# Kernel tuning notes

Measured on AMD Instinct MI355X. Metric: run time of the kernel, lower is better.

The kernel has to match this reference:

```python
import jax, jax.numpy as jnp
import numpy as np
from jax import lax

# Paraformer-large streaming decoder dims
L, H, DFF, NH, DK, K, V, T, S, CKV, LB = 16, 512, 2048, 4, 128, 11, 8404, 64, 2048, 256, 256


def _ln(x, g, b, eps=1e-5):
    m = jnp.mean(x, axis=-1, keepdims=True)
    var = jnp.mean((x - m) ** 2, axis=-1, keepdims=True)
    return (x - m) * lax.rsqrt(var + eps) * g + b


def setup_inputs() -> dict:
    key = jax.random.key(0)
    ks = jax.random.split(key, 20)
    w = lambda k, shp: jax.random.normal(k, shp, jnp.float32) * 0.02
    return {
        "encoder_out": jax.random.normal(ks[0], (1, S, H), jnp.float32),
        "list_frame": jax.random.normal(ks[1], (1, T, H), jnp.float32),
        "fsmn_cache": jax.random.normal(ks[2], (L, 1, H, K - 1), jnp.float32),
        "key_cache": jax.random.normal(ks[3], (L, NH, DK, CKV), jnp.float32),
        "value_cache": jax.random.normal(ks[4], (L, NH, CKV, DK), jnp.float32),
        "norm1_g": jnp.ones((L, H)), "norm1_b": jnp.zeros((L, H)),
        "norm2_g": jnp.ones((L, H)), "norm2_b": jnp.zeros((L, H)),
        "norm3_g": jnp.ones((L, H)), "norm3_b": jnp.zeros((L, H)),
        "ffn_norm_g": jnp.ones((L, DFF)), "ffn_norm_b": jnp.zeros((L, DFF)),
        "w1": w(ks[5], (L, H, DFF)), "b1": jnp.zeros((L, DFF)),
        "w2": w(ks[6], (L, DFF, H)),  # bias-free in FunASR DecoderSANM
        "fsmn_w": w(ks[7], (L, H, K)),  # depthwise conv, groups=H, no bias
        "qw": w(ks[8], (L, H, H)), "qb": jnp.zeros((L, H)),
        "kvw": w(ks[9], (L, H, 2 * H)), "kvb": jnp.zeros((L, 2 * H)),
        "ow": w(ks[10], (L, H, H)), "ob": jnp.zeros((L, H)),
        "d3_norm1_g": jnp.ones((H,)), "d3_norm1_b": jnp.zeros((H,)),
        "d3_w1": w(ks[11], (H, DFF)), "d3_b1": jnp.zeros((DFF,)),
        "d3_ffn_norm_g": jnp.ones((DFF,)), "d3_ffn_norm_b": jnp.zeros((DFF,)),
        "d3_w2": w(ks[12], (DFF, H)),
        "after_norm_g": jnp.ones((H,)), "after_norm_b": jnp.zeros((H,)),
        "out_w": w(ks[13], (H, V)), "out_b": jnp.zeros((V,)),
        "list_frame_len": T,
    }


def reference(encoder_out, list_frame, fsmn_cache, key_cache, value_cache,
              norm1_g, norm1_b, norm2_g, norm2_b, norm3_g, norm3_b,
              ffn_norm_g, ffn_norm_b, w1, b1, w2, fsmn_w, qw, qb, kvw, kvb, ow, ob,
              d3_norm1_g, d3_norm1_b, d3_w1, d3_b1, d3_ffn_norm_g, d3_ffn_norm_b, d3_w2,
              after_norm_g, after_norm_b, out_w, out_b, list_frame_len):
    enc = encoder_out[0]  # [S, H]
    scale = DK ** -0.5

    def layer_fn(lf, p):
        (fc, kc, vc, n1g, n1b, n2g, n2b, n3g, n3b, fng, fnb,
         W1, B1, W2, FW, QW, QB, KVW, KVB, OW, OB) = p
        residual = lf
        y = _ln(lf, n1g, n1b)
        y = _ln(jax.nn.relu(y @ W1 + B1), fng, fnb) @ W2
        y = _ln(y, n2g, n2b)
        # cache concat; slice [look_back:] with look_back = -(K-1)-T keeps all K-1+T cols
        x_cat = jnp.concatenate([fc, jnp.swapaxes(y, 1, 2)], axis=-1)  # [1, H, K-1+T]
        conv = lax.conv_general_dilated(
            x_cat, FW[:, None, :], (1,), 'VALID',
            dimension_numbers=('NCH', 'OIH', 'NCH'), feature_group_count=H)  # [1, H, T]
        x = jnp.swapaxes(conv, 1, 2) + y + residual
        residual = x
        q = (_ln(x, n3g, n3b)[0] @ QW + QB).reshape(-1, NH, DK).transpose(1, 0, 2) * scale  # [h, T, dk]
        kv = enc @ KVW + KVB  # [S, 2H]
        k = kv[:, :H].reshape(-1, NH, DK).transpose(1, 2, 0)  # [h, dk, S]
        v = kv[:, H:].reshape(-1, NH, DK).transpose(1, 0, 2)  # [h, S, dk]
        k = jnp.concatenate([kc, k], axis=2)  # [h, dk, CKV+S]
        v = jnp.concatenate([vc, v], axis=1)  # [h, CKV+S, dk]
        attn = jax.nn.softmax(jnp.einsum('htd,hds->hts', q, k), axis=-1)
        ctx = jnp.einsum('hts,hsd->htd', attn, v).transpose(1, 0, 2).reshape(1, -1, H)
        lf = residual + ctx @ OW + OB
        return lf, (x_cat, k[:, :, -LB:], v[:, -LB:, :])

    layer_params = (fsmn_cache, key_cache, value_cache, norm1_g, norm1_b, norm2_g, norm2_b,
                    norm3_g, norm3_b, ffn_norm_g, ffn_norm_b, w1, b1, w2, fsmn_w,
                    qw, qb, kvw, kvb, ow, ob)
    lf, (save_fsmn, save_keys, save_values) = lax.scan(layer_fn, list_frame, layer_params)
    x = _ln(lf, d3_norm1_g, d3_norm1_b)
    x = _ln(jax.nn.relu(x @ d3_w1 + d3_b1), d3_ffn_norm_g, d3_ffn_norm_b) @ d3_w2
    logits = _ln(x, after_norm_g, after_norm_b) @ out_w + out_b
    max_logit_ids = jnp.argmax(logits, axis=-1).astype(jnp.int32)
    return save_fsmn, save_keys, save_values, max_logit_ids
```

## Files before the change

kernel.cpp:

```cpp
#include <hip/hip_runtime.h>

constexpr int LAY = 16, HID = 512, FF = 2048, NHD = 4, DKH = 128, KW = 11,
              VOC = 8404, TT = 64, SEQ = 2048, LBN = 256;

#define SWZ(row, e) ((e) ^ ((((row) >> 2) & 7) << 2))

__global__ void diag_k(float* __restrict__ p, float v) { p[threadIdx.x] = v; }

__global__ __launch_bounds__(256) void redln_k(
    const float* __restrict__ P, int N, int nch,
    const float* __restrict__ bias, const float* __restrict__ res, int relu,
    const float* __restrict__ g, const float* __restrict__ b,
    float* __restrict__ out1, float* __restrict__ out2) {
  __shared__ float buf[2048];
  __shared__ float red[256];
  const int m = blockIdx.x, tid = threadIdx.x;
  float s = 0.f;
  for (int n = tid; n < N; n += 256) {
    const float* p = P + (size_t)m * N + n;
    float v = 0.f;
    for (int c = 0; c < nch; ++c) v += p[(size_t)c * 64 * N];
    if (bias) v += bias[n];
    if (res) v += res[(size_t)m * N + n];
    if (relu) v = fmaxf(v, 0.f);
    if (out1) out1[(size_t)m * N + n] = v;
    buf[n] = v; s += v;
  }
  red[tid] = s; __syncthreads();
  for (int st = 128; st > 0; st >>= 1) { if (tid < st) red[tid] += red[tid + st]; __syncthreads(); }
  const float mean = red[0] / N;
  __syncthreads();
  float vs = 0.f;
  for (int n = tid; n < N; n += 256) { float d = buf[n] - mean; vs += d * d; }
  red[tid] = vs; __syncthreads();
  for (int st = 128; st > 0; st >>= 1) { if (tid < st) red[tid] += red[tid + st]; __syncthreads(); }
  const float inv = rsqrtf(red[0] / N + 1e-5f);
  for (int n = tid; n < N; n += 256)
    out2[(size_t)m * N + n] = (buf[n] - mean) * inv * g[n] + b[n];
}

__global__ __launch_bounds__(256) void gemm_nn(
    const float* __restrict__ A, int lda, long sA,
    const float* __restrict__ B, int ldb, long sB,
    float* __restrict__ C, int ldc, long sC,
    const float* __restrict__ bias,
    const float* __restrict__ res, int ldres,
    int N, int Kd, int flags, int nch,
    float* __restrict__ part, long pzs, int coff,
    int aCh, long aChS) {
  __shared__ float As[64][64];
  __shared__ float Bs[64][64];
  const int tid = threadIdx.x;
  const int lr = tid >> 4, lc = tid & 15;
  const int bn = blockIdx.x * 64;
  const int chunk = blockIdx.y;
  const int z = blockIdx.z;
  A += (long)z * sA; B += (long)z * sB; C += (long)z * sC;
  float acc[4][4] = {};
  const int ktiles = Kd >> 6;
  const int fa = (lc & 7) << 2;
  for (int kt = chunk; kt < ktiles; kt += nch) {
    const int k0 = kt << 6;
    __syncthreads();
#pragma unroll
    for (int i = 0; i < 4; ++i) {
      const int r = lr + 16 * i;
      const float* ap = A + (size_t)r * lda + k0 + lc * 4;
      float4 av = *(const float4*)ap;
      for (int c = 1; c < aCh; ++c) {
        const float4 t2 = *(const float4*)(ap + (size_t)c * aChS);
        av.x += t2.x; av.y += t2.y; av.z += t2.z; av.w += t2.w;
      }
      As[lc * 4 + 0][r ^ fa] = av.x; As[lc * 4 + 1][r ^ fa] = av.y;
      As[lc * 4 + 2][r ^ fa] = av.z; As[lc * 4 + 3][r ^ fa] = av.w;
      const int n = bn + lc * 4;
      const float* bp = B + (size_t)(k0 + r) * ldb + n;
      float4 bv;
      if (n + 3 < N) bv = *(const float4*)bp;
      else {
        bv.x = (n + 0 < N) ? bp[0] : 0.f;
        bv.y = (n + 1 < N) ? bp[1] : 0.f;
        bv.z = (n + 2 < N) ? bp[2] : 0.f;
        bv.w = (n + 3 < N) ? bp[3] : 0.f;
      }
      *(float4*)(&Bs[r][SWZ(r, lc * 4)]) = bv;
    }
    __syncthreads();
#pragma unroll 8
    for (int kk = 0; kk < 64; ++kk) {
      const int fk = ((kk >> 2) & 7) << 2;
      const float4 a = *(const float4*)(&As[kk][(lr * 4) ^ fk]);
      const float4 b = *(const float4*)(&Bs[kk][(lc * 4) ^ fk]);
      acc[0][0] += a.x * b.x; acc[0][1] += a.x * b.y; acc[0][2] += a.x * b.z; acc[0][3] += a.x * b.w;
      acc[1][0] += a.y * b.x; acc[1][1] += a.y * b.y; acc[1][2] += a.y * b.z; acc[1][3] += a.y * b.w;
      acc[2][0] += a.z * b.x; acc[2][1] += a.z * b.y; acc[2][2] += a.z * b.z; acc[2][3] += a.z * b.w;
      acc[3][0] += a.w * b.x; acc[3][1] += a.w * b.y; acc[3][2] += a.w * b.z; acc[3][3] += a.w * b.w;
    }
  }
  if (part) {
    float* P = part + (size_t)z * pzs + (size_t)(coff + chunk) * 64 * N;
#pragma unroll
    for (int i = 0; i < 4; ++i) {
      const int m = lr * 4 + i;
#pragma unroll
      for (int j = 0; j < 4; ++j) P[(size_t)m * N + bn + lc * 4 + j] = acc[i][j];
    }
    return;
  }
#pragma unroll
  for (int i = 0; i < 4; ++i) {
    const int m = lr * 4 + i;
#pragma unroll
    for (int j = 0; j < 4; ++j) {
      const int n = bn + lc * 4 + j;
      if (n < N) {
        float v = acc[i][j];
        if (bias) v += bias[n];
        if (res) v += res[(size_t)m * ldres + n];
        if (flags & 2) v += C[(size_t)m * ldc + n];
        if (flags & 1) v = fmaxf(v, 0.f);
        C[(size_t)m * ldc + n] = v;
      }
    }
  }
}

__global__ __launch_bounds__(256) void red_k(
    const float* __restrict__ P, float* __restrict__ out,
    int N, int nch, long pzs, int outld, int zoff,
    const float* __restrict__ bias, const float* __restrict__ res,
    const float* __restrict__ rsv, const float* __restrict__ bvv,
    int relu, int total) {
  const int idx = blockIdx.x * 256 + threadIdx.x;
  if (idx >= total) return;
  const int z = idx / (64 * N);
  const int rem = idx - z * 64 * N;
  const int t = rem / N;
  const int n = rem - t * N;
  const float* p = P + (size_t)z * pzs + (size_t)t * N + n;
  float s = 0.f;
  for (int c = 0; c < nch; ++c) s += p[(size_t)c * 64 * N];
  const int oc = z * zoff + n;
  if (bias) s += bias[oc];
  if (res) s += res[(size_t)t * outld + oc];
  if (rsv) s += rsv[z * 64 + t] * bvv[oc];
  if (relu) s = fmaxf(s, 0.f);
  out[(size_t)t * outld + oc] = s;
}

__global__ __launch_bounds__(256) void gemm_nt(
    const float* __restrict__ A, int lda, long sA,
    const float* __restrict__ B, int ldb, long sB,
    float* __restrict__ C, int ldc, long sC,
    int N, int Kd, int nch, float* __restrict__ part) {
  __shared__ float As[64][64];
  __shared__ float Bs[64][64];
  const int tid = threadIdx.x;
  const int lr = tid >> 4, lc = tid & 15;
  const int bn = blockIdx.x * 64;
  const int chunk = blockIdx.y;
  const int z = blockIdx.z;
  A += (long)z * sA; B += (long)z * sB; C += (long)z * sC;
  float acc[4][4] = {};
  const int ktiles = Kd >> 6;
  const int fa = (lc & 7) << 2;
  for (int kt = chunk; kt < ktiles; kt += nch) {
    const int k0 = kt << 6;
    __syncthreads();
#pragma unroll
    for (int i = 0; i < 4; ++i) {
      const int r = lr + 16 * i;
      const float4 av = *(const float4*)(A + (size_t)r * lda + k0 + lc * 4);
      As[lc * 4 + 0][r ^ fa] = av.x; As[lc * 4 + 1][r ^ fa] = av.y;
      As[lc * 4 + 2][r ^ fa] = av.z; As[lc * 4 + 3][r ^ fa] = av.w;
      const float4 bv = *(const float4*)(B + (size_t)(bn + r) * ldb + k0 + lc * 4);
      Bs[lc * 4 + 0][r ^ fa] = bv.x; Bs[lc * 4 + 1][r ^ fa] = bv.y;
      Bs[lc * 4 + 2][r ^ fa] = bv.z; Bs[lc * 4 + 3][r ^ fa] = bv.w;
    }
    __syncthreads();
#pragma unroll 8
    for (int kk = 0; kk < 64; ++kk) {
      const int fk = ((kk >> 2) & 7) << 2;
      const float4 a = *(const float4*)(&As[kk][(lr * 4) ^ fk]);
      const float4 b = *(const float4*)(&Bs[kk][(lc * 4) ^ fk]);
      acc[0][0] += a.x * b.x; acc[0][1] += a.x * b.y; acc[0][2] += a.x * b.z; acc[0][3] += a.x * b.w;
      acc[1][0] += a.y * b.x; acc[1][1] += a.y * b.y; acc[1][2] += a.y * b.z; acc[1][3] += a.y * b.w;
      acc[2][0] += a.z * b.x; acc[2][1] += a.z * b.y; acc[2][2] += a.z * b.z; acc[2][3] += a.z * b.w;
      acc[3][0] += a.w * b.x; acc[3][1] += a.w * b.y; acc[3][2] += a.w * b.z; acc[3][3] += a.w * b.w;
    }
  }
  if (chunk == 0) {
#pragma unroll
    for (int i = 0; i < 4; ++i)
#pragma unroll
      for (int j = 0; j < 4; ++j)
        C[(size_t)(lr * 4 + i) * ldc + bn + lc * 4 + j] = acc[i][j];
  } else {
    float* P = part + (size_t)z * (64L * SEQ) + (size_t)(chunk - 1) * 64 * SEQ * NHD;
#pragma unroll
    for (int i = 0; i < 4; ++i)
#pragma unroll
      for (int j = 0; j < 4; ++j)
        P[(size_t)(lr * 4 + i) * SEQ + bn + lc * 4 + j] = acc[i][j];
  }
}

__global__ __launch_bounds__(256) void attn1_k(
    const float* __restrict__ qpart, const float* __restrict__ qbi_l,
    const float* __restrict__ Wkv, const float* __restrict__ kcl,
    float* __restrict__ qp, float* __restrict__ sc,
    int ckv, int sct) {
  __shared__ float As[64][64];
  __shared__ float Bs[64][64];
  const int tid = threadIdx.x;
  const int lr = tid >> 4, lc = tid & 15;
  const int h = blockIdx.z;
  const bool isQp = blockIdx.x < 8;
  const int bn = (isQp ? blockIdx.x : blockIdx.x - 8) * 64;
  const int fa = (lc & 7) << 2;
  float acc[4][4] = {};
  for (int k0 = 0; k0 < DKH; k0 += 64) {
    __syncthreads();
#pragma unroll
    for (int i = 0; i < 4; ++i) {
      const int r = lr + 16 * i;
      const float* ap = qpart + (size_t)r * HID + h * DKH + k0 + lc * 4;
      float4 av = *(const float4*)ap;
      for (int c = 1; c < 8; ++c) {
        const float4 t2 = *(const float4*)(ap + (size_t)c * 64 * HID);
        av.x += t2.x; av.y += t2.y; av.z += t2.z; av.w += t2.w;
      }
      const float4 bb = *(const float4*)(qbi_l + h * DKH + k0 + lc * 4);
      av.x += bb.x; av.y += bb.y; av.z += bb.z; av.w += bb.w;
      As[lc * 4 + 0][r ^ fa] = av.x; As[lc * 4 + 1][r ^ fa] = av.y;
      As[lc * 4 + 2][r ^ fa] = av.z; As[lc * 4 + 3][r ^ fa] = av.w;
      if (isQp) {
        const float4 bv = *(const float4*)(Wkv + (size_t)(bn + r) * (2 * HID) + h * DKH + k0 + lc * 4);
        Bs[lc * 4 + 0][r ^ fa] = bv.x; Bs[lc * 4 + 1][r ^ fa] = bv.y;
        Bs[lc * 4 + 2][r ^ fa] = bv.z; Bs[lc * 4 + 3][r ^ fa] = bv.w;
      } else {
        const float4 bv = *(const float4*)(kcl + ((size_t)h * DKH + k0 + r) * ckv + bn + lc * 4);
        *(float4*)(&Bs[r][SWZ(r, lc * 4)]) = bv;
      }
    }
    __syncthreads();
#pragma unroll 8
    for (int kk = 0; kk < 64; ++kk) {
      const int fk = ((kk >> 2) & 7) << 2;
      const float4 a = *(const float4*)(&As[kk][(lr * 4) ^ fk]);
      const float4 b = *(const float4*)(&Bs[kk][(lc * 4) ^ fk]);
      acc[0][0] += a.x * b.x; acc[0][1] += a.x * b.y; acc[0][2] += a.x * b.z; acc[0][3] += a.x * b.w;
      acc[1][0] += a.y * b.x; acc[1][1] += a.y * b.y; acc[1][2] += a.y * b.z; acc[1][3] += a.y * b.w;
      acc[2][0] += a.z * b.x; acc[2][1] += a.z * b.y; acc[2][2] += a.z * b.z; acc[2][3] += a.z * b.w;
      acc[3][0] += a.w * b.x; acc[3][1] += a.w * b.y; acc[3][2] += a.w * b.z; acc[3][3] += a.w * b.w;
    }
  }
  if (isQp) {
    float* C = qp + (size_t)h * TT * HID;
#pragma unroll
    for (int i = 0; i < 4; ++i)
#pragma unroll
      for (int j = 0; j < 4; ++j)
        C[(size_t)(lr * 4 + i) * HID + bn + lc * 4 + j] = acc[i][j];
  } else {
    float* C = sc + (size_t)h * TT * sct;
#pragma unroll
    for (int i = 0; i < 4; ++i)
#pragma unroll
      for (int j = 0; j < 4; ++j)
        C[(size_t)(lr * 4 + i) * sct + bn + lc * 4 + j] = acc[i][j];
  }
}

__global__ __launch_bounds__(256) void attn2_k(
    const float* __restrict__ sc, const float* __restrict__ vcl,
    const float* __restrict__ enc,
    float* __restrict__ part, float* __restrict__ partE,
    int ckv, int sct, int ncho, long pzc) {
  __shared__ float As[64][64];
  __shared__ float Bs[64][64];
  const int tid = threadIdx.x;
  const int lr = tid >> 4, lc = tid & 15;
  const int h = blockIdx.z;
  const int by = blockIdx.y;
  const bool isOld = blockIdx.x < 2;
  if (isOld && by >= ncho) return;
  if (!isOld && by >= 8) return;
  const float* A;
  const float* Bb;
  int lda, ldb, N, ktiles, nch, bn;
  float* P;
  if (isOld) {
    A = sc + (size_t)h * TT * sct;  lda = sct;
    Bb = vcl + (size_t)h * ckv * DKH; ldb = DKH;
    N = DKH; ktiles = ckv >> 6; nch = ncho; bn = blockIdx.x * 64;
    P = part + (size_t)h * pzc + (size_t)by * 64 * DKH;
  } else {
    A = sc + ckv + (size_t)h * TT * sct; lda = sct;
    Bb = enc; ldb = HID;
    N = HID; ktiles = SEQ >> 6; nch = 8; bn = (blockIdx.x - 2) * 64;
    P = partE + (size_t)h * (8L * 64 * HID) + (size_t)by * 64 * HID;
  }
  const int fa = (lc & 7) << 2;
  float acc[4][4] = {};
  for (int kt = by; kt < ktiles; kt += nch) {
    const int k0 = kt << 6;
    __syncthreads();
#pragma unroll
    for (int i = 0; i < 4; ++i) {
      const int r = lr + 16 * i;
      const float4 av = *(const float4*)(A + (size_t)r * lda + k0 + lc * 4);
      As[lc * 4 + 0][r ^ fa] = av.x; As[lc * 4 + 1][r ^ fa] = av.y;
      As[lc * 4 + 2][r ^ fa] = av.z; As[lc * 4 + 3][r ^ fa] = av.w;
      const float4 bv = *(const float4*)(Bb + (size_t)(k0 + r) * ldb + bn + lc * 4);
      *(float4*)(&Bs[r][SWZ(r, lc * 4)]) = bv;
    }
    __syncthreads();
#pragma unroll 8
    for (int kk = 0; kk < 64; ++kk) {
      const int fk = ((kk >> 2) & 7) << 2;
      const float4 a = *(const float4*)(&As[kk][(lr * 4) ^ fk]);
      const float4 b = *(const float4*)(&Bs[kk][(lc * 4) ^ fk]);
      acc[0][0] += a.x * b.x; acc[0][1] += a.x * b.y; acc[0][2] += a.x * b.z; acc[0][3] += a.x * b.w;
      acc[1][0] += a.y * b.x; acc[1][1] += a.y * b.y; acc[1][2] += a.y * b.z; acc[1][3] += a.y * b.w;
      acc[2][0] += a.z * b.x; acc[2][1] += a.z * b.y; acc[2][2] += a.z * b.z; acc[2][3] += a.z * b.w;
      acc[3][0] += a.w * b.x; acc[3][1] += a.w * b.y; acc[3][2] += a.w * b.z; acc[3][3] += a.w * b.w;
    }
  }
#pragma unroll
  for (int i = 0; i < 4; ++i)
#pragma unroll
    for (int j = 0; j < 4; ++j)
      P[(size_t)(lr * 4 + i) * N + bn + lc * 4 + j] = acc[i][j];
}

__global__ __launch_bounds__(256) void fsmnln_k(
    const float* __restrict__ y4, const float* __restrict__ lfin,
    const float* __restrict__ cache, const float* __restrict__ fw,
    const float* __restrict__ g, const float* __restrict__ b,
    float* __restrict__ xb, float* __restrict__ xcat,
    float* __restrict__ y1out) {
  __shared__ float buf[HID];
  __shared__ float red[256];
  const int t = blockIdx.x, tid = threadIdx.x;
  float s = 0.f;
  for (int h = tid; h < HID; h += 256) {
    float conv = 0.f;
#pragma unroll
    for (int k = 0; k < KW; ++k) {
      const int j = t + k;
      const float xcv = (j < KW - 1) ? cache[h * (KW - 1) + j]
                                     : y4[(size_t)(j - (KW - 1)) * HID + h];
      conv += xcv * fw[h * KW + k];
    }
    const float yv = y4[(size_t)t * HID + h];
    const float x = conv + yv + lfin[(size_t)t * HID + h];
    xb[(size_t)t * HID + h] = x;
    buf[h] = x; s += x;
    xcat[h * (KW - 1 + TT) + (KW - 1) + t] = yv;
    if (t == 0) {
      for (int j2 = 0; j2 < KW - 1; ++j2)
        xcat[h * (KW - 1 + TT) + j2] = cache[h * (KW - 1) + j2];
    }
  }
  red[tid] = s; __syncthreads();
  for (int st = 128; st > 0; st >>= 1) { if (tid < st) red[tid] += red[tid + st]; __syncthreads(); }
  const float mean = red[0] / HID;
  __syncthreads();
  float vs = 0.f;
  for (int h = tid; h < HID; h += 256) { float d = buf[h] - mean; vs += d * d; }
  red[tid] = vs; __syncthreads();
  for (int st = 128; st > 0; st >>= 1) { if (tid < st) red[tid] += red[tid + st]; __syncthreads(); }
  const float inv = rsqrtf(red[0] / HID + 1e-5f);
  for (int h = tid; h < HID; h += 256)
    y1out[(size_t)t * HID + h] = (buf[h] - mean) * inv * g[h] + b[h];
}

__global__ __launch_bounds__(256) void softmax_k(
    float* __restrict__ sc, float* __restrict__ rs,
    const float* __restrict__ qpart, const float* __restrict__ qbi_l,
    const float* __restrict__ kb, const float* __restrict__ partN,
    int cols, int newStart, float alpha) {
  __shared__ float srow[8192];
  __shared__ float red[256];
  const int tid = threadIdx.x;
  const int row = blockIdx.x;
  const int h = row >> 6, t = row & 63;
  sc += (size_t)row * cols;
  const float* pn = partN + (size_t)h * 64 * SEQ + (size_t)t * SEQ;
  float qv = 0.f;
  if (tid < DKH) {
    const float* qp0 = qpart + (size_t)t * HID + h * DKH + tid;
    float q = qp0[0];
    for (int c = 1; c < 8; ++c) q += qp0[(size_t)c * 64 * HID];
    q += qbi_l[h * DKH + tid];
    qv = q * kb[h * DKH + tid];
  }
  red[tid] = qv; __syncthreads();
  for (int st = 64; st > 0; st >>= 1) { if (tid < st) red[tid] += red[tid + st]; __syncthreads(); }
  const float qcv = red[0];
  __syncthreads();
  float m = -3.4e38f;
  for (int c = tid; c < cols; c += 256) {
    float v = sc[c];
    if (c >= newStart) v += pn[c - newStart] + qcv;
    v *= alpha;
    srow[c] = v; m = fmaxf(m, v);
  }
  red[tid] = m; __syncthreads();
  for (int st = 128; st > 0; st >>= 1) { if (tid < st) red[tid] = fmaxf(red[tid], red[tid + st]); __syncthreads(); }
  m = red[0]; __syncthreads();
  float s = 0.f;
  for (int c = tid; c < cols; c += 256) {
    const float e = __expf(srow[c] - m);
    srow[c] = e; s += e;
  }
  red[tid] = s; __syncthreads();
  for (int st = 128; st > 0; st >>= 1) { if (tid < st) red[tid] += red[tid + st]; __syncthreads(); }
  const float inv = 1.f / red[0];
  float ns = 0.f;
  for (int c = tid; c < cols; c += 256) {
    const float p = srow[c] * inv; sc[c] = p;
    if (c >= newStart) ns += p;
  }
  __syncthreads();
  red[tid] = ns; __syncthreads();
  for (int st = 128; st > 0; st >>= 1) { if (tid < st) red[tid] += red[tid + st]; __syncthreads(); }
  if (tid == 0) rs[row] = red[0];
}

__global__ __launch_bounds__(256) void argmax_k(const float* __restrict__ lg,
                                                float* __restrict__ out) {
  __shared__ float vs[256];
  __shared__ int ix[256];
  const int tid = threadIdx.x;
  lg += (size_t)blockIdx.x * VOC;
  float bm = -3.4e38f;
  int bi = 0;
  for (int c = tid; c < VOC; c += 256) { float v = lg[c]; if (v > bm) { bm = v; bi = c; } }
  vs[tid] = bm; ix[tid] = bi; __syncthreads();
  for (int st = 128; st > 0; st >>= 1) {
    if (tid < st) {
      if (vs[tid + st] > vs[tid] || (vs[tid + st] == vs[tid] && ix[tid + st] < ix[tid])) {
        vs[tid] = vs[tid + st]; ix[tid] = ix[tid + st];
      }
    }
    __syncthreads();
  }
  if (tid == 0) out[blockIdx.x] = (float)ix[0];
}

__global__ __launch_bounds__(256) void kvsave_k(const float* __restrict__ enc,
                                                const float* __restrict__ kvw,
                                                const float* __restrict__ kvb,
                                                float* __restrict__ keys,
                                                float* __restrict__ vals) {
  __shared__ float As[64][64];
  __shared__ float Bs[64][64];
  const int tid = threadIdx.x;
  const int lr = tid >> 4, lc = tid & 15;
  const int bn = blockIdx.x * 64, bm = blockIdx.y * 64;
  const int l = blockIdx.z;
  const float* W = kvw + (size_t)l * HID * 2 * HID;
  const int fa = (lc & 7) << 2;
  float acc[4][4] = {};
  for (int k0 = 0; k0 < HID; k0 += 64) {
    __syncthreads();
#pragma unroll
    for (int i = 0; i < 4; ++i) {
      const int r = lr + 16 * i;
      const float4 av =
          *(const float4*)(enc + (size_t)(SEQ - LBN + bm + r) * HID + k0 + lc * 4);
      As[lc * 4 + 0][r ^ fa] = av.x; As[lc * 4 + 1][r ^ fa] = av.y;
      As[lc * 4 + 2][r ^ fa] = av.z; As[lc * 4 + 3][r ^ fa] = av.w;
      const float4 bv = *(const float4*)(W + (size_t)(k0 + r) * (2 * HID) + bn + lc * 4);
      *(float4*)(&Bs[r][SWZ(r, lc * 4)]) = bv;
    }
    __syncthreads();
#pragma unroll 8
    for (int kk = 0; kk < 64; ++kk) {
      const int fk = ((kk >> 2) & 7) << 2;
      const float4 a = *(const float4*)(&As[kk][(lr * 4) ^ fk]);
      const float4 b = *(const float4*)(&Bs[kk][(lc * 4) ^ fk]);
      acc[0][0] += a.x * b.x; acc[0][1] += a.x * b.y; acc[0][2] += a.x * b.z; acc[0][3] += a.x * b.w;
      acc[1][0] += a.y * b.x; acc[1][1] += a.y * b.y; acc[1][2] += a.y * b.z; acc[1][3] += a.y * b.w;
      acc[2][0] += a.z * b.x; acc[2][1] += a.z * b.y; acc[2][2] += a.z * b.z; acc[2][3] += a.z * b.w;
      acc[3][0] += a.w * b.x; acc[3][1] += a.w * b.y; acc[3][2] += a.w * b.z; acc[3][3] += a.w * b.w;
    }
  }
#pragma unroll
  for (int i = 0; i < 4; ++i) {
    const int m = bm + lr * 4 + i;
#pragma unroll
    for (int j = 0; j < 4; ++j) {
      const int n = bn + lc * 4 + j;
      const float v = acc[i][j] + kvb[(size_t)l * 2 * HID + n];
      if (n < 512) {
        const int h = n >> 7, d = n & 127;
        keys[(((size_t)l * NHD + h) * DKH + d) * LBN + m] = v;
      } else {
        const int c = n - 512, h = c >> 7, d = c & 127;
        vals[(((size_t)l * NHD + h) * LBN + m) * DKH + d] = v;
      }
    }
  }
}

extern "C" void kernel_launch(void* const* d_in, const int* in_sizes, int n_in,
                              void* d_out, int out_size, void* d_ws, size_t ws_size,
                              hipStream_t stream) {
  static const int EXPECT[34] = {
      1048576, 32768, 81920, -1, -1,
      8192, 8192, 8192, 8192, 8192, 8192,
      32768, 32768,
      16777216, 32768, 16777216, 90112,
      4194304, 8192, 8388608, 16384, 4194304, 8192,
      512, 512, 1048576, 2048, 2048, 2048, 1048576,
      512, 512, 4302848, 8404};
  if (out_size != 4800576) {
    diag_k<<<1, 64, 0, stream>>>((float*)d_out, 9800000.f);
    return;
  }
  float* out_fsmn = (float*)d_out;
  float* out_keys = out_fsmn + (size_t)LAY * HID * (KW - 1 + TT);
  float* out_vals = out_keys + (size_t)LAY * NHD * DKH * LBN;
  float* out_ids  = out_vals + (size_t)LAY * NHD * LBN * DKH;
  if (n_in < 34) {
    diag_k<<<1, 64, 0, stream>>>(out_ids, 9900000.f);
    return;
  }
  for (int i = 0; i < 34; ++i) {
    if (EXPECT[i] >= 0 && in_sizes[i] != EXPECT[i]) {
      diag_k<<<1, 64, 0, stream>>>(out_ids, (float)((i + 1) * 100000));
      return;
    }
  }
  const long per = (long)LAY * NHD * DKH;
  const long ckl = (long)in_sizes[3] / per;
  if ((long)in_sizes[3] != ckl * per || in_sizes[4] != in_sizes[3] ||
      ckl <= 0 || (ckl & 63) != 0 || ckl > 6144) {
    diag_k<<<1, 64, 0, stream>>>(out_fsmn, (float)in_sizes[3]);
    return;
  }
  if (ws_size < (size_t)3145728 * 4) {
    diag_k<<<1, 64, 0, stream>>>(out_fsmn, 1.0e6f + (float)(ws_size >> 20));
    return;
  }
  const int ckv = (int)ckl;
  const int sct = ckv + SEQ;
  const long TS = (long)TT * sct;
  const int ncho = (ckv / 64 < 8) ? (ckv / 64) : 8;

  const float* enc    = (const float*)d_in[0];
  const float* lfrm   = (const float*)d_in[1];
  const float* fcache = (const float*)d_in[2];
  const float* kcache = (const float*)d_in[3];
  const float* vcache = (const float*)d_in[4];
  const float* n1g = (const float*)d_in[5];  const float* n1b = (const float*)d_in[6];
  const float* n2g = (const float*)d_in[7];  const float* n2b = (const float*)d_in[8];
  const float* n3g = (const float*)d_in[9];  const float* n3b = (const float*)d_in[10];
  const float* fng = (const float*)d_in[11]; const float* fnb = (const float*)d_in[12];
  const float* w1  = (const float*)d_in[13]; const float* b1  = (const float*)d_in[14];
  const float* w2  = (const float*)d_in[15];
  const float* fw  = (const float*)d_in[16];
  const float* qw  = (const float*)d_in[17]; const float* qbi  = (const float*)d_in[18];
  const float* kvw = (const float*)d_in[19]; const float* kvbi = (const float*)d_in[20];
  const float* ow  = (const float*)d_in[21]; const float* obi  = (const float*)d_in[22];
  const float* d3n1g = (const float*)d_in[23]; const float* d3n1b = (const float*)d_in[24];
  const float* d3w1  = (const float*)d_in[25]; const float* d3b1  = (const float*)d_in[26];
  const float* d3fng = (const float*)d_in[27]; const float* d3fnb = (const float*)d_in[28];
  const float* d3w2  = (const float*)d_in[29];
  const float* ang   = (const float*)d_in[30]; const float* anb = (const float*)d_in[31];
  const float* outw  = (const float*)d_in[32]; const float* outb = (const float*)d_in[33];

  float* sc  = out_keys;
  float* ov  = out_vals;
  float* lf  = ov + 0;
  float* y1  = ov + 32768;
  float* y4  = ov + 98304;
  float* xb  = ov + 131072;
  float* ctx = ov + 196608;
  float* y2  = ov + 360448;
  float* qp  = ov + 491520;
  float* rs  = ov + 753920;
  float* lg  = ov + 754176;
  float* wsf   = (float*)d_ws;
  float* part  = wsf;
  float* partE = wsf + 1048576;
  float* partN = wsf + 2097152;

  const float alpha = 0.08838834764831845f;
  const long TH = (long)TT * HID;
  const long pz_ctx = (long)(ncho + 4) * 64 * DKH;

  redln_k<<<TT, 256, 0, stream>>>(lfrm, HID, 1, nullptr, nullptr, 0,
                                  n1g, n1b, lf, y1);

  for (int l = 0; l < LAY; ++l) {
    const float* Wkv = kvw + (size_t)l * HID * 2 * HID;
    const float* Bkv = kvbi + (size_t)l * 2 * HID;
    const float* qbi_l = qbi + (size_t)l * HID;
    gemm_nn<<<dim3(32, 8, 1), 256, 0, stream>>>(
        y1, HID, 0, w1 + (size_t)l * HID * FF, FF, 0, nullptr, 0, 0,
        nullptr, nullptr, 0, FF, HID, 0, 8, part, 0, 0, 1, 0);
    redln_k<<<TT, 256, 0, stream>>>(part, FF, 8, b1 + (size_t)l * FF, nullptr, 1,
                                    fng + (size_t)l * FF, fnb + (size_t)l * FF,
                                    nullptr, y2);
    gemm_nn<<<dim3(8, 32, 1), 256, 0, stream>>>(
        y2, FF, 0, w2 + (size_t)l * FF * HID, HID, 0, nullptr, 0, 0,
        nullptr, nullptr, 0, HID, FF, 0, 32, part, 0, 0, 1, 0);
    redln_k<<<TT, 256, 0, stream>>>(part, HID, 32, nullptr, nullptr, 0,
                                    n2g + l * HID, n2b + l * HID, nullptr, y4);
    fsmnln_k<<<TT, 256, 0, stream>>>(y4, lf, fcache + (size_t)l * HID * (KW - 1),
                                     fw + (size_t)l * HID * KW,
                                     n3g + l * HID, n3b + l * HID,
                                     xb, out_fsmn + (size_t)l * HID * (KW - 1 + TT), y1);
    gemm_nn<<<dim3(8, 8, 1), 256, 0, stream>>>(
        y1, HID, 0, qw + (size_t)l * HID * HID, HID, 0, nullptr, 0, 0,
        nullptr, nullptr, 0, HID, HID, 0, 8, part, 0, 0, 1, 0);
    attn1_k<<<dim3(8 + ckv / 64, 1, NHD), 256, 0, stream>>>(
        part, qbi_l, Wkv, kcache + (size_t)l * NHD * DKH * ckv, qp, sc, ckv, sct);
    gemm_nt<<<dim3(32, 2, NHD), 256, 0, stream>>>(
        qp, HID, TH, enc, HID, 0, sc + ckv, sct, TS, SEQ, HID, 2, partN);
    softmax_k<<<NHD * TT, 256, 0, stream>>>(sc, rs, part, qbi_l, Bkv, partN,
                                            sct, ckv, alpha);
    attn2_k<<<dim3(10, 8, NHD), 256, 0, stream>>>(
        sc, vcache + (size_t)l * NHD * ckv * DKH, enc, part, partE,
        ckv, sct, ncho, pz_ctx);
    gemm_nn<<<dim3(2, 4, NHD), 256, 0, stream>>>(
        partE, HID, 8L * 64 * HID, Wkv + HID, 2 * HID, DKH, nullptr, 0, 0,
        nullptr, nullptr, 0, DKH, HID, 0, 4, part, pz_ctx, ncho, 8, 64L * HID);
    red_k<<<128, 256, 0, stream>>>(part, ctx, DKH, ncho + 4, pz_ctx, HID, DKH,
                                   nullptr, nullptr, rs, Bkv + HID, 0, NHD * TT * DKH);
    gemm_nn<<<dim3(8, 8, 1), 256, 0, stream>>>(
        ctx, HID, 0, ow + (size_t)l * HID * HID, HID, 0, nullptr, 0, 0,
        nullptr, nullptr, 0, HID, HID, 0, 8, part, 0, 0, 1, 0);
    const float* ng = (l + 1 < LAY) ? n1g + (l + 1) * HID : d3n1g;
    const float* nb = (l + 1 < LAY) ? n1b + (l + 1) * HID : d3n1b;
    redln_k<<<TT, 256, 0, stream>>>(part, HID, 8, obi + (size_t)l * HID, xb, 0,
                                    ng, nb, lf, y1);
  }

  gemm_nn<<<dim3(32, 8, 1), 256, 0, stream>>>(
      y1, HID, 0, d3w1, FF, 0, nullptr, 0, 0, nullptr, nullptr, 0,
      FF, HID, 0, 8, part, 0, 0, 1, 0);
  redln_k<<<TT, 256, 0, stream>>>(part, FF, 8, d3b1, nullptr, 1,
                                  d3fng, d3fnb, nullptr, y2);
  gemm_nn<<<dim3(8, 32, 1), 256, 0, stream>>>(
      y2, FF, 0, d3w2, HID, 0, nullptr, 0, 0, nullptr, nullptr, 0,
      HID, FF, 0, 32, part, 0, 0, 1, 0);
  redln_k<<<TT, 256, 0, stream>>>(part, HID, 32, nullptr, nullptr, 0,
                                  ang, anb, nullptr, y4);
  gemm_nn<<<dim3((VOC + 63) / 64, 1, 1), 256, 0, stream>>>(
      y4, HID, 0, outw, VOC, 0, lg, VOC, 0, outb, nullptr, 0,
      VOC, HID, 0, 1, nullptr, 0, 0, 1, 0);
  argmax_k<<<TT, 256, 0, stream>>>(lg, out_ids);

  kvsave_k<<<dim3(2 * HID / 64, LBN / 64, LAY), 256, 0, stream>>>(
      enc, kvw, kvbi, out_keys, out_vals);
}
```

Measured before the change: 3.015 ms.

## Pack four independent 256-thread tiles into each 1024-thread block

Each kernel now launches blocks of 256x4 threads. Every threadIdx.y slice works on its own tile, chunk or row with private shared memory, and grids shrink by four. This cuts the number of blocks scheduled, perhaps to fit an occupancy or dispatch pattern. Shared memory per block grows to 128KB for the GEMM kernels, which may limit residency to one block per CU. The __syncthreads calls now span all four slices, so each slice waits on the others. A dedicated gemm_vx is added for the vocab projection, and the unused res and flags paths are removed.

```diff
diff --git a/kernel.cpp b/kernel.cpp
--- a/kernel.cpp
+++ b/kernel.cpp
@@ -7,14 +7,15 @@
 
 __global__ void diag_k(float* __restrict__ p, float v) { p[threadIdx.x] = v; }
 
-__global__ __launch_bounds__(256) void redln_k(
+__global__ __launch_bounds__(1024) void redln_k(
     const float* __restrict__ P, int N, int nch,
     const float* __restrict__ bias, const float* __restrict__ res, int relu,
     const float* __restrict__ g, const float* __restrict__ b,
     float* __restrict__ out1, float* __restrict__ out2) {
-  __shared__ float buf[2048];
-  __shared__ float red[256];
-  const int m = blockIdx.x, tid = threadIdx.x;
+  __shared__ float buf[4][2048];
+  __shared__ float red[4][256];
+  const int ty = threadIdx.y, tid = threadIdx.x;
+  const int m = blockIdx.x * 4 + ty;
   float s = 0.f;
   for (int n = tid; n < N; n += 256) {
     const float* p = P + (size_t)m * N + n;
@@ -24,36 +25,37 @@
     if (res) v += res[(size_t)m * N + n];
     if (relu) v = fmaxf(v, 0.f);
     if (out1) out1[(size_t)m * N + n] = v;
-    buf[n] = v; s += v;
-  }
-  red[tid] = s; __syncthreads();
-  for (int st = 128; st > 0; st >>= 1) { if (tid < st) red[tid] += red[tid + st]; __syncthreads(); }
-  const float mean = red[0] / N;
+    buf[ty][n] = v; s += v;
+  }
+  red[ty][tid] = s; __syncthreads();
+  for (int st = 128; st > 0; st >>= 1) { if (tid < st) red[ty][tid] += red[ty][tid + st]; __syncthreads(); }
+  const float mean = red[ty][0] / N;
   __syncthreads();
   float vs = 0.f;
-  for (int n = tid; n < N; n += 256) { float d = buf[n] - mean; vs += d * d; }
-  red[tid] = vs; __syncthreads();
-  for (int st = 128; st > 0; st >>= 1) { if (tid < st) red[tid] += red[tid + st]; __syncthreads(); }
-  const float inv = rsqrtf(red[0] / N + 1e-5f);
+  for (int n = tid; n < N; n += 256) { float d = buf[ty][n] - mean; vs += d * d; }
+  red[ty][tid] = vs; __syncthreads();
+  for (int st = 128; st > 0; st >>= 1) { if (tid < st) red[ty][tid] += red[ty][tid + st]; __syncthreads(); }
+  const float inv = rsqrtf(red[ty][0] / N + 1e-5f);
   for (int n = tid; n < N; n += 256)
-    out2[(size_t)m * N + n] = (buf[n] - mean) * inv * g[n] + b[n];
-}
-
-__global__ __launch_bounds__(256) void gemm_nn(
+    out2[(size_t)m * N + n] = (buf[ty][n] - mean) * inv * g[n] + b[n];
+}
+
+__global__ __launch_bounds__(1024) void gemm_nn(
     const float* __restrict__ A, int lda, long sA,
     const float* __restrict__ B, int ldb, long sB,
     float* __restrict__ C, int ldc, long sC,
     const float* __restrict__ bias,
-    const float* __restrict__ res, int ldres,
     int N, int Kd, int flags, int nch,
     float* __restrict__ part, long pzs, int coff,
     int aCh, long aChS) {
-  __shared__ float As[64][64];
-  __shared__ float Bs[64][64];
-  const int tid = threadIdx.x;
+  __shared__ float As[4][64][64];
+  __shared__ float Bs[4][64][64];
+  const int ty = threadIdx.y, tid = threadIdx.x;
   const int lr = tid >> 4, lc = tid & 15;
   const int bn = blockIdx.x * 64;
-  const int chunk = blockIdx.y;
+  int chunk = blockIdx.y * 4 + ty;
+  const int valid = chunk < nch;
+  if (!valid) chunk = nch - 1;
   const int z = blockIdx.z;
   A += (long)z * sA; B += (long)z * sB; C += (long)z * sC;
   float acc[4][4] = {};
@@ -71,8 +73,8 @@
         const float4 t2 = *(const float4*)(ap + (size_t)c * aChS);
         av.x += t2.x; av.y += t2.y; av.z += t2.z; av.w += t2.w;
       }
-      As[lc * 4 + 0][r ^ fa] = av.x; As[lc * 4 + 1][r ^ fa] = av.y;
-      As[lc * 4 + 2][r ^ fa] = av.z; As[lc * 4 + 3][r ^ fa] = av.w;
+      As[ty][lc * 4 + 0][r ^ fa] = av.x; As[ty][lc * 4 + 1][r ^ fa] = av.y;
+      As[ty][lc * 4 + 2][r ^ fa] = av.z; As[ty][lc * 4 + 3][r ^ fa] = av.w;
       const int n = bn + lc * 4;
       const float* bp = B + (size_t)(k0 + r) * ldb + n;
       float4 bv;
@@ -83,20 +85,21 @@
         bv.z = (n + 2 < N) ? bp[2] : 0.f;
         bv.w = (n + 3 < N) ? bp[3] : 0.f;
       }
-      *(float4*)(&Bs[r][SWZ(r, lc * 4)]) = bv;
+      *(float4*)(&Bs[ty][r][SWZ(r, lc * 4)]) = bv;
     }
     __syncthreads();
 #pragma unroll 8
     for (int kk = 0; kk < 64; ++kk) {
       const int fk = ((kk >> 2) & 7) << 2;
-      const float4 a = *(const float4*)(&As[kk][(lr * 4) ^ fk]);
-      const float4 b = *(const float4*)(&Bs[kk][(lc * 4) ^ fk]);
+      const float4 a = *(const float4*)(&As[ty][kk][(lr * 4) ^ fk]);
+      const float4 b = *(const float4*)(&Bs[ty][kk][(lc * 4) ^ fk]);
       acc[0][0] += a.x * b.x; acc[0][1] += a.x * b.y; acc[0][2] += a.x * b.z; acc[0][3] += a.x * b.w;
       acc[1][0] += a.y * b.x; acc[1][1] += a.y * b.y; acc[1][2] += a.y * b.z; acc[1][3] += a.y * b.w;
       acc[2][0] += a.z * b.x; acc[2][1] += a.z * b.y; acc[2][2] += a.z * b.z; acc[2][3] += a.z * b.w;
       acc[3][0] += a.w * b.x; acc[3][1] += a.w * b.y; acc[3][2] += a.w * b.z; acc[3][3] += a.w * b.w;
     }
   }
+  if (!valid) return;
   if (part) {
     float* P = part + (size_t)z * pzs + (size_t)(coff + chunk) * 64 * N;
 #pragma unroll
@@ -116,8 +119,6 @@
       if (n < N) {
         float v = acc[i][j];
         if (bias) v += bias[n];
-        if (res) v += res[(size_t)m * ldres + n];
-        if (flags & 2) v += C[(size_t)m * ldc + n];
         if (flags & 1) v = fmaxf(v, 0.f);
         C[(size_t)m * ldc + n] = v;
       }
@@ -125,13 +126,70 @@
   }
 }
 
-__global__ __launch_bounds__(256) void red_k(
+__global__ __launch_bounds__(1024) void gemm_vx(
+    const float* __restrict__ A, int lda,
+    const float* __restrict__ B, int ldb,
+    float* __restrict__ C, int ldc,
+    const float* __restrict__ bias, int N, int Kd, int ntx) {
+  __shared__ float As[4][64][64];
+  __shared__ float Bs[4][64][64];
+  const int ty = threadIdx.y, tid = threadIdx.x;
+  const int lr = tid >> 4, lc = tid & 15;
+  int tile = blockIdx.x * 4 + ty;
+  const int valid = tile < ntx;
+  if (!valid) tile = 0;
+  const int bn = tile * 64;
+  const int fa = (lc & 7) << 2;
+  float acc[4][4] = {};
+  for (int k0 = 0; k0 < Kd; k0 += 64) {
+    __syncthreads();
+#pragma unroll
+    for (int i = 0; i < 4; ++i) {
+      const int r = lr + 16 * i;
+      const float4 av = *(const float4*)(A + (size_t)r * lda + k0 + lc * 4);
+      As[ty][lc * 4 + 0][r ^ fa] = av.x; As[ty][lc * 4 + 1][r ^ fa] = av.y;
+      As[ty][lc * 4 + 2][r ^ fa] = av.z; As[ty][lc * 4 + 3][r ^ fa] = av.w;
+      const int n = bn + lc * 4;
+      const float* bp = B + (size_t)(k0 + r) * ldb + n;
+      float4 bv;
+      if (n + 3 < N) bv = *(const float4*)bp;
+      else {
+        bv.x = (n + 0 < N) ? bp[0] : 0.f;
+        bv.y = (n + 1 < N) ? bp[1] : 0.f;
+        bv.z = (n + 2 < N) ? bp[2] : 0.f;
+        bv.w = (n + 3 < N) ? bp[3] : 0.f;
+      }
+      *(float4*)(&Bs[ty][r][SWZ(r, lc * 4)]) = bv;
+    }
+    __syncthreads();
+#pragma unroll 8
+    for (int kk = 0; kk < 64; ++kk) {
+      const int fk = ((kk >> 2) & 7) << 2;
+      const float4 a = *(const float4*)(&As[ty][kk][(lr * 4) ^ fk]);
+      const float4 b = *(const float4*)(&Bs[ty][kk][(lc * 4) ^ fk]);
+      acc[0][0] += a.x * b.x; acc[0][1] += a.x * b.y; acc[0][2] += a.x * b.z; acc[0][3] += a.x * b.w;
+      acc[1][0] += a.y * b.x; acc[1][1] += a.y * b.y; acc[1][2] += a.y * b.z; acc[1][3] += a.y * b.w;
+      acc[2][0] += a.z * b.x; acc[2][1] += a.z * b.y; acc[2][2] += a.z * b.z; acc[2][3] += a.z * b.w;
+      acc[3][0] += a.w * b.x; acc[3][1] += a.w * b.y; acc[3][2] += a.w * b.z; acc[3][3] += a.w * b.w;
+    }
+  }
+  if (!valid) return;
+#pragma unroll
+  for (int i = 0; i < 4; ++i) {
+    const int m = lr * 4 + i;
+#pragma unroll
+    for (int j = 0; j < 4; ++j) {
+      const int n = bn + lc * 4 + j;
+      if (n < N) C[(size_t)m * ldc + n] = acc[i][j] + bias[n];
+    }
+  }
+}
+
+__global__ __launch_bounds__(1024) void red_k(
     const float* __restrict__ P, float* __restrict__ out,
     int N, int nch, long pzs, int outld, int zoff,
-    const float* __restrict__ bias, const float* __restrict__ res,
-    const float* __restrict__ rsv, const float* __restrict__ bvv,
-    int relu, int total) {
-  const int idx = blockIdx.x * 256 + threadIdx.x;
+    const float* __restrict__ rsv, const float* __restrict__ bvv, int total) {
+  const int idx = blockIdx.x * 1024 + threadIdx.x;
   if (idx >= total) return;
   const int z = idx / (64 * N);
   const int rem = idx - z * 64 * N;
@@ -141,23 +199,23 @@
   float s = 0.f;
   for (int c = 0; c < nch; ++c) s += p[(size_t)c * 64 * N];
   const int oc = z * zoff + n;
-  if (bias) s += bias[oc];
-  if (res) s += res[(size_t)t * outld + oc];
   if (rsv) s += rsv[z * 64 + t] * bvv[oc];
-  if (relu) s = fmaxf(s, 0.f);
   out[(size_t)t * outld + oc] = s;
 }
 
-__global__ __launch_bounds__(256) void gemm_nt(
+__global__ __launch_bounds__(1024) void gemm_nt(
     const float* __restrict__ A, int lda, long sA,
     const float* __restrict__ B, int ldb, long sB,
     float* __restrict__ C, int ldc, long sC,
     int N, int Kd, int nch, float* __restrict__ part) {
-  __shared__ float As[64][64];
-  __shared__ float Bs[64][64];
-  const int tid = threadIdx.x;
+  __shared__ float As[4][64][64];
+  __shared__ float Bs[4][64][64];
+  const int ty = threadIdx.y, tid = threadIdx.x;
   const int lr = tid >> 4, lc = tid & 15;
-  const int bn = blockIdx.x * 64;
+  int tile = blockIdx.x * 4 + ty;
+  const int valid = tile * 64 < N;
+  if (!valid) tile = 0;
+  const int bn = tile * 64;
   const int chunk = blockIdx.y;
   const int z = blockIdx.z;
   A += (long)z * sA; B += (long)z * sB; C += (long)z * sC;
@@ -171,24 +229,25 @@
     for (int i = 0; i < 4; ++i) {
       const int r = lr + 16 * i;
       const float4 av = *(const float4*)(A + (size_t)r * lda + k0 + lc * 4);
-      As[lc * 4 + 0][r ^ fa] = av.x; As[lc * 4 + 1][r ^ fa] = av.y;
-      As[lc * 4 + 2][r ^ fa] = av.z; As[lc * 4 + 3][r ^ fa] = av.w;
+      As[ty][lc * 4 + 0][r ^ fa] = av.x; As[ty][lc * 4 + 1][r ^ fa] = av.y;
+      As[ty][lc * 4 + 2][r ^ fa] = av.z; As[ty][lc * 4 + 3][r ^ fa] = av.w;
       const float4 bv = *(const float4*)(B + (size_t)(bn + r) * ldb + k0 + lc * 4);
-      Bs[lc * 4 + 0][r ^ fa] = bv.x; Bs[lc * 4 + 1][r ^ fa] = bv.y;
-      Bs[lc * 4 + 2][r ^ fa] = bv.z; Bs[lc * 4 + 3][r ^ fa] = bv.w;
+      Bs[ty][lc * 4 + 0][r ^ fa] = bv.x; Bs[ty][lc * 4 + 1][r ^ fa] = bv.y;
+      Bs[ty][lc * 4 + 2][r ^ fa] = bv.z; Bs[ty][lc * 4 + 3][r ^ fa] = bv.w;
     }
     __syncthreads();
 #pragma unroll 8
     for (int kk = 0; kk < 64; ++kk) {
       const int fk = ((kk >> 2) & 7) << 2;
-      const float4 a = *(const float4*)(&As[kk][(lr * 4) ^ fk]);
-      const float4 b = *(const float4*)(&Bs[kk][(lc * 4) ^ fk]);
+      const float4 a = *(const float4*)(&As[ty][kk][(lr * 4) ^ fk]);
+      const float4 b = *(const float4*)(&Bs[ty][kk][(lc * 4) ^ fk]);
       acc[0][0] += a.x * b.x; acc[0][1] += a.x * b.y; acc[0][2] += a.x * b.z; acc[0][3] += a.x * b.w;
       acc[1][0] += a.y * b.x; acc[1][1] += a.y * b.y; acc[1][2] += a.y * b.z; acc[1][3] += a.y * b.w;
       acc[2][0] += a.z * b.x; acc[2][1] += a.z * b.y; acc[2][2] += a.z * b.z; acc[2][3] += a.z * b.w;
       acc[3][0] += a.w * b.x; acc[3][1] += a.w * b.y; acc[3][2] += a.w * b.z; acc[3][3] += a.w * b.w;
     }
   }
+  if (!valid) return;
   if (chunk == 0) {
 #pragma unroll
     for (int i = 0; i < 4; ++i)
@@ -205,18 +264,21 @@
   }
 }
 
-__global__ __launch_bounds__(256) void attn1_k(
+__global__ __launch_bounds__(1024) void attn1_k(
     const float* __restrict__ qpart, const float* __restrict__ qbi_l,
     const float* __restrict__ Wkv, const float* __restrict__ kcl,
     float* __restrict__ qp, float* __restrict__ sc,
     int ckv, int sct) {
-  __shared__ float As[64][64];
-  __shared__ float Bs[64][64];
-  const int tid = threadIdx.x;
+  __shared__ float As[4][64][64];
+  __shared__ float Bs[4][64][64];
+  const int ty = threadIdx.y, tid = threadIdx.x;
   const int lr = tid >> 4, lc = tid & 15;
   const int h = blockIdx.z;
-  const bool isQp = blockIdx.x < 8;
-  const int bn = (isQp ? blockIdx.x : blockIdx.x - 8) * 64;
+  int tile = blockIdx.x * 4 + ty;
+  const int valid = tile < 8 + ckv / 64;
+  if (!valid) tile = 0;
+  const bool isQp = tile < 8;
+  const int bn = (isQp ? tile : tile - 8) * 64;
   const int fa = (lc & 7) << 2;
   float acc[4][4] = {};
   for (int k0 = 0; k0 < DKH; k0 += 64) {
@@ -232,29 +294,30 @@
       }
       const float4 bb = *(const float4*)(qbi_l + h * DKH + k0 + lc * 4);
       av.x += bb.x; av.y += bb.y; av.z += bb.z; av.w += bb.w;
-      As[lc * 4 + 0][r ^ fa] = av.x; As[lc * 4 + 1][r ^ fa] = av.y;
-      As[lc * 4 + 2][r ^ fa] = av.z; As[lc * 4 + 3][r ^ fa] = av.w;
+      As[ty][lc * 4 + 0][r ^ fa] = av.x; As[ty][lc * 4 + 1][r ^ fa] = av.y;
+      As[ty][lc * 4 + 2][r ^ fa] = av.z; As[ty][lc * 4 + 3][r ^ fa] = av.w;
       if (isQp) {
         const float4 bv = *(const float4*)(Wkv + (size_t)(bn + r) * (2 * HID) + h * DKH + k0 + lc * 4);
-        Bs[lc * 4 + 0][r ^ fa] = bv.x; Bs[lc * 4 + 1][r ^ fa] = bv.y;
-        Bs[lc * 4 + 2][r ^ fa] = bv.z; Bs[lc * 4 + 3][r ^ fa] = bv.w;
+        Bs[ty][lc * 4 + 0][r ^ fa] = bv.x; Bs[ty][lc * 4 + 1][r ^ fa] = bv.y;
+        Bs[ty][lc * 4 + 2][r ^ fa] = bv.z; Bs[ty][lc * 4 + 3][r ^ fa] = bv.w;
       } else {
         const float4 bv = *(const float4*)(kcl + ((size_t)h * DKH + k0 + r) * ckv + bn + lc * 4);
-        *(float4*)(&Bs[r][SWZ(r, lc * 4)]) = bv;
+        *(float4*)(&Bs[ty][r][SWZ(r, lc * 4)]) = bv;
       }
     }
     __syncthreads();
 #pragma unroll 8
     for (int kk = 0; kk < 64; ++kk) {
       const int fk = ((kk >> 2) & 7) << 2;
-      const float4 a = *(const float4*)(&As[kk][(lr * 4) ^ fk]);
-      const float4 b = *(const float4*)(&Bs[kk][(lc * 4) ^ fk]);
+      const float4 a = *(const float4*)(&As[ty][kk][(lr * 4) ^ fk]);
+      const float4 b = *(const float4*)(&Bs[ty][kk][(lc * 4) ^ fk]);
       acc[0][0] += a.x * b.x; acc[0][1] += a.x * b.y; acc[0][2] += a.x * b.z; acc[0][3] += a.x * b.w;
       acc[1][0] += a.y * b.x; acc[1][1] += a.y * b.y; acc[1][2] += a.y * b.z; acc[1][3] += a.y * b.w;
       acc[2][0] += a.z * b.x; acc[2][1] += a.z * b.y; acc[2][2] += a.z * b.z; acc[2][3] += a.z * b.w;
       acc[3][0] += a.w * b.x; acc[3][1] += a.w * b.y; acc[3][2] += a.w * b.z; acc[3][3] += a.w * b.w;
     }
   }
+  if (!valid) return;
   if (isQp) {
     float* C = qp + (size_t)h * TT * HID;
 #pragma unroll
@@ -272,35 +335,39 @@
   }
 }
 
-__global__ __launch_bounds__(256) void attn2_k(
+__global__ __launch_bounds__(1024) void attn2_k(
     const float* __restrict__ sc, const float* __restrict__ vcl,
     const float* __restrict__ enc,
     float* __restrict__ part, float* __restrict__ partE,
     int ckv, int sct, int ncho, long pzc) {
-  __shared__ float As[64][64];
-  __shared__ float Bs[64][64];
-  const int tid = threadIdx.x;
+  __shared__ float As[4][64][64];
+  __shared__ float Bs[4][64][64];
+  const int ty = threadIdx.y, tid = threadIdx.x;
   const int lr = tid >> 4, lc = tid & 15;
   const int h = blockIdx.z;
   const int by = blockIdx.y;
-  const bool isOld = blockIdx.x < 2;
+  const bool isOld = blockIdx.x == 0;
   if (isOld && by >= ncho) return;
   if (!isOld && by >= 8) return;
+  int xt, valid;
   const float* A;
   const float* Bb;
-  int lda, ldb, N, ktiles, nch, bn;
+  int lda, ldb, N, ktiles, nch;
   float* P;
   if (isOld) {
+    xt = ty; valid = xt < 2; if (!valid) xt = 0;
     A = sc + (size_t)h * TT * sct;  lda = sct;
     Bb = vcl + (size_t)h * ckv * DKH; ldb = DKH;
-    N = DKH; ktiles = ckv >> 6; nch = ncho; bn = blockIdx.x * 64;
+    N = DKH; ktiles = ckv >> 6; nch = ncho;
     P = part + (size_t)h * pzc + (size_t)by * 64 * DKH;
   } else {
+    xt = (blockIdx.x - 1) * 4 + ty; valid = 1;
     A = sc + ckv + (size_t)h * TT * sct; lda = sct;
     Bb = enc; ldb = HID;
-    N = HID; ktiles = SEQ >> 6; nch = 8; bn = (blockIdx.x - 2) * 64;
+    N = HID; ktiles = SEQ >> 6; nch = 8;
     P = partE + (size_t)h * (8L * 64 * HID) + (size_t)by * 64 * HID;
   }
+  const int bn = xt * 64;
   const int fa = (lc & 7) << 2;
   float acc[4][4] = {};
   for (int kt = by; kt < ktiles; kt += nch) {
@@ -310,23 +377,24 @@
     for (int i = 0; i < 4; ++i) {
       const int r = lr + 16 * i;
       const float4 av = *(const float4*)(A + (size_t)r * lda + k0 + lc * 4);
-      As[lc * 4 + 0][r ^ fa] = av.x; As[lc * 4 + 1][r ^ fa] = av.y;
-      As[lc * 4 + 2][r ^ fa] = av.z; As[lc * 4 + 3][r ^ fa] = av.w;
+      As[ty][lc * 4 + 0][r ^ fa] = av.x; As[ty][lc * 4 + 1][r ^ fa] = av.y;
+      As[ty][lc * 4 + 2][r ^ fa] = av.z; As[ty][lc * 4 + 3][r ^ fa] = av.w;
       const float4 bv = *(const float4*)(Bb + (size_t)(k0 + r) * ldb + bn + lc * 4);
-      *(float4*)(&Bs[r][SWZ(r, lc * 4)]) = bv;
+      *(float4*)(&Bs[ty][r][SWZ(r, lc * 4)]) = bv;
     }
     __syncthreads();
 #pragma unroll 8
     for (int kk = 0; kk < 64; ++kk) {
       const int fk = ((kk >> 2) & 7) << 2;
-      const float4 a = *(const float4*)(&As[kk][(lr * 4) ^ fk]);
-      const float4 b = *(const float4*)(&Bs[kk][(lc * 4) ^ fk]);
+      const float4 a = *(const float4*)(&As[ty][kk][(lr * 4) ^ fk]);
+      const float4 b = *(const float4*)(&Bs[ty][kk][(lc * 4) ^ fk]);
       acc[0][0] += a.x * b.x; acc[0][1] += a.x * b.y; acc[0][2] += a.x * b.z; acc[0][3] += a.x * b.w;
       acc[1][0] += a.y * b.x; acc[1][1] += a.y * b.y; acc[1][2] += a.y * b.z; acc[1][3] += a.y * b.w;
       acc[2][0] += a.z * b.x; acc[2][1] += a.z * b.y; acc[2][2] += a.z * b.z; acc[2][3] += a.z * b.w;
       acc[3][0] += a.w * b.x; acc[3][1] += a.w * b.y; acc[3][2] += a.w * b.z; acc[3][3] += a.w * b.w;
     }
   }
+  if (!valid) return;
 #pragma unroll
   for (int i = 0; i < 4; ++i)
 #pragma unroll
@@ -334,15 +402,16 @@
       P[(size_t)(lr * 4 + i) * N + bn + lc * 4 + j] = acc[i][j];
 }
 
-__global__ __launch_bounds__(256) void fsmnln_k(
+__global__ __launch_bounds__(1024) void fsmnln_k(
     const float* __restrict__ y4, const float* __restrict__ lfin,
     const float* __restrict__ cache, const float* __restrict__ fw,
     const float* __restrict__ g, const float* __restrict__ b,
     float* __restrict__ xb, float* __restrict__ xcat,
     float* __restrict__ y1out) {
-  __shared__ float buf[HID];
-  __shared__ float red[256];
-  const int t = blockIdx.x, tid = threadIdx.x;
+  __shared__ float buf[4][HID];
+  __shared__ float red[4][256];
+  const int ty = threadIdx.y, tid = threadIdx.x;
+  const int t = blockIdx.x * 4 + ty;
   float s = 0.f;
   for (int h = tid; h < HID; h += 256) {
     float conv = 0.f;
@@ -356,35 +425,35 @@
     const float yv = y4[(size_t)t * HID + h];
     const float x = conv + yv + lfin[(size_t)t * HID + h];
     xb[(size_t)t * HID + h] = x;
-    buf[h] = x; s += x;
+    buf[ty][h] = x; s += x;
     xcat[h * (KW - 1 + TT) + (KW - 1) + t] = yv;
     if (t == 0) {
       for (int j2 = 0; j2 < KW - 1; ++j2)
         xcat[h * (KW - 1 + TT) + j2] = cache[h * (KW - 1) + j2];
     }
   }
-  red[tid] = s; __syncthreads();
-  for (int st = 128; st > 0; st >>= 1) { if (tid < st) red[tid] += red[tid + st]; __syncthreads(); }
-  const float mean = red[0] / HID;
+  red[ty][tid] = s; __syncthreads();
+  for (int st = 128; st > 0; st >>= 1) { if (tid < st) red[ty][tid] += red[ty][tid + st]; __syncthreads(); }
+  const float mean = red[ty][0] / HID;
   __syncthreads();
   float vs = 0.f;
-  for (int h = tid; h < HID; h += 256) { float d = buf[h] - mean; vs += d * d; }
-  red[tid] = vs; __syncthreads();
-  for (int st = 128; st > 0; st >>= 1) { if (tid < st) red[tid] += red[tid + st]; __syncthreads(); }
-  const float inv = rsqrtf(red[0] / HID + 1e-5f);
+  for (int h = tid; h < HID; h += 256) { float d = buf[ty][h] - mean; vs += d * d; }
+  red[ty][tid] = vs; __syncthreads();
+  for (int st = 128; st > 0; st >>= 1) { if (tid < st) red[ty][tid] += red[ty][tid + st]; __syncthreads(); }
+  const float inv = rsqrtf(red[ty][0] / HID + 1e-5f);
   for (int h = tid; h < HID; h += 256)
-    y1out[(size_t)t * HID + h] = (buf[h] - mean) * inv * g[h] + b[h];
-}
-
-__global__ __launch_bounds__(256) void softmax_k(
+    y1out[(size_t)t * HID + h] = (buf[ty][h] - mean) * inv * g[h] + b[h];
+}
+
+__global__ __launch_bounds__(1024) void softmax_k(
     float* __restrict__ sc, float* __restrict__ rs,
     const float* __restrict__ qpart, const float* __restrict__ qbi_l,
     const float* __restrict__ kb, const float* __restrict__ partN,
     int cols, int newStart, float alpha) {
-  __shared__ float srow[8192];
-  __shared__ float red[256];
-  const int tid = threadIdx.x;
-  const int row = blockIdx.x;
+  __shared__ float srow[4][8192];
+  __shared__ float red[4][256];
+  const int ty = threadIdx.y, tid = threadIdx.x;
+  const int row = blockIdx.x * 4 + ty;
   const int h = row >> 6, t = row & 63;
   sc += (size_t)row * cols;
   const float* pn = partN + (size_t)h * 64 * SEQ + (size_t)t * SEQ;
@@ -396,70 +465,73 @@
     q += qbi_l[h * DKH + tid];
     qv = q * kb[h * DKH + tid];
   }
-  red[tid] = qv; __syncthreads();
-  for (int st = 64; st > 0; st >>= 1) { if (tid < st) red[tid] += red[tid + st]; __syncthreads(); }
-  const float qcv = red[0];
+  red[ty][tid] = qv; __syncthreads();
+  for (int st = 64; st > 0; st >>= 1) { if (tid < st) red[ty][tid] += red[ty][tid + st]; __syncthreads(); }
+  const float qcv = red[ty][0];
   __syncthreads();
   float m = -3.4e38f;
   for (int c = tid; c < cols; c += 256) {
     float v = sc[c];
     if (c >= newStart) v += pn[c - newStart] + qcv;
     v *= alpha;
-    srow[c] = v; m = fmaxf(m, v);
-  }
-  red[tid] = m; __syncthreads();
-  for (int st = 128; st > 0; st >>= 1) { if (tid < st) red[tid] = fmaxf(red[tid], red[tid + st]); __syncthreads(); }
-  m = red[0]; __syncthreads();
+    srow[ty][c] = v; m = fmaxf(m, v);
+  }
+  red[ty][tid] = m; __syncthreads();
+  for (int st = 128; st > 0; st >>= 1) { if (tid < st) red[ty][tid] = fmaxf(red[ty][tid], red[ty][tid + st]); __syncthreads(); }
+  m = red[ty][0]; __syncthreads();
   float s = 0.f;
   for (int c = tid; c < cols; c += 256) {
-    const float e = __expf(srow[c] - m);
-    srow[c] = e; s += e;
-  }
-  red[tid] = s; __syncthreads();
-  for (int st = 128; st > 0; st >>= 1) { if (tid < st) red[tid] += red[tid + st]; __syncthreads(); }
-  const float inv = 1.f / red[0];
+    const float e = __expf(srow[ty][c] - m);
+    srow[ty][c] = e; s += e;
+  }
+  red[ty][tid] = s; __syncthreads();
+  for (int st = 128; st > 0; st >>= 1) { if (tid < st) red[ty][tid] += red[ty][tid + st]; __syncthreads(); }
+  const float inv = 1.f / red[ty][0];
   float ns = 0.f;
   for (int c = tid; c < cols; c += 256) {
-    const float p = srow[c] * inv; sc[c] = p;
+    const float p = srow[ty][c] * inv; sc[c] = p;
     if (c >= newStart) ns += p;
   }
   __syncthreads();
-  red[tid] = ns; __syncthreads();
-  for (int st = 128; st > 0; st >>= 1) { if (tid < st) red[tid] += red[tid + st]; __syncthreads(); }
-  if (tid == 0) rs[row] = red[0];
-}
-
-__global__ __launch_bounds__(256) void argmax_k(const float* __restrict__ lg,
-                                                float* __restrict__ out) {
-  __shared__ float vs[256];
-  __shared__ int ix[256];
-  const int tid = threadIdx.x;
-  lg += (size_t)blockIdx.x * VOC;
+  red[ty][tid] = ns; __syncthreads();
+  for (int st = 128; st > 0; st >>= 1) { if (tid < st) red[ty][tid] += red[ty][tid + st]; __syncthreads(); }
+  if (tid == 0) rs[row] = red[ty][0];
+}
+
+__global__ __launch_bounds__(1024) void argmax_k(const float* __restrict__ lg,
+                                                 float* __restrict__ out) {
+  __shared__ float vs[4][256];
+  __shared__ int ix[4][256];
+  const int ty = threadIdx.y, tid = threadIdx.x;
+  const int row = blockIdx.x * 4 + ty;
+  lg += (size_t)row * VOC;
   float bm = -3.4e38f;
   int bi = 0;
   for (int c = tid; c < VOC; c += 256) { float v = lg[c]; if (v > bm) { bm = v; bi = c; } }
-  vs[tid] = bm; ix[tid] = bi; __syncthreads();
+  vs[ty][tid] = bm; ix[ty][tid] = bi; __syncthreads();
   for (int st = 128; st > 0; st >>= 1) {
     if (tid < st) {
-      if (vs[tid + st] > vs[tid] || (vs[tid + st] == vs[tid] && ix[tid + st] < ix[tid])) {
-        vs[tid] = vs[tid + st]; ix[tid] = ix[tid + st];
+      if (vs[ty][tid + st] > vs[ty][tid] ||
+          (vs[ty][tid + st] == vs[ty][tid] && ix[ty][tid + st] < ix[ty][tid])) {
+        vs[ty][tid] = vs[ty][tid + st]; ix[ty][tid] = ix[ty][tid + st];
       }
     }
     __syncthreads();
   }
-  if (tid == 0) out[blockIdx.x] = (float)ix[0];
-}
-
-__global__ __launch_bounds__(256) void kvsave_k(const float* __restrict__ enc,
-                                                const float* __restrict__ kvw,
-                                                const float* __restrict__ kvb,
-                                                float* __restrict__ keys,
-                                                float* __restrict__ vals) {
-  __shared__ float As[64][64];
-  __shared__ float Bs[64][64];
-  const int tid = threadIdx.x;
+  if (tid == 0) out[row] = (float)ix[ty][0];
+}
+
+__global__ __launch_bounds__(1024) void kvsave_k(const float* __restrict__ enc,
+                                                 const float* __restrict__ kvw,
+                                                 const float* __restrict__ kvb,
+                                                 float* __restrict__ keys,
+                                                 float* __restrict__ vals) {
+  __shared__ float As[4][64][64];
+  __shared__ float Bs[4][64][64];
+  const int ty = threadIdx.y, tid = threadIdx.x;
   const int lr = tid >> 4, lc = tid & 15;
-  const int bn = blockIdx.x * 64, bm = blockIdx.y * 64;
+  const int bn = (blockIdx.x * 4 + ty) * 64;
+  const int bm = blockIdx.y * 64;
   const int l = blockIdx.z;
   const float* W = kvw + (size_t)l * HID * 2 * HID;
   const int fa = (lc & 7) << 2;
@@ -471,17 +543,17 @@
       const int r = lr + 16 * i;
       const float4 av =
           *(const float4*)(enc + (size_t)(SEQ - LBN + bm + r) * HID + k0 + lc * 4);
-      As[lc * 4 + 0][r ^ fa] = av.x; As[lc * 4 + 1][r ^ fa] = av.y;
-      As[lc * 4 + 2][r ^ fa] = av.z; As[lc * 4 + 3][r ^ fa] = av.w;
+      As[ty][lc * 4 + 0][r ^ fa] = av.x; As[ty][lc * 4 + 1][r ^ fa] = av.y;
+      As[ty][lc * 4 + 2][r ^ fa] = av.z; As[ty][lc * 4 + 3][r ^ fa] = av.w;
       const float4 bv = *(const float4*)(W + (size_t)(k0 + r) * (2 * HID) + bn + lc * 4);
-      *(float4*)(&Bs[r][SWZ(r, lc * 4)]) = bv;
+      *(float4*)(&Bs[ty][r][SWZ(r, lc * 4)]) = bv;
     }
     __syncthreads();
 #pragma unroll 8
     for (int kk = 0; kk < 64; ++kk) {
       const int fk = ((kk >> 2) & 7) << 2;
-      const float4 a = *(const float4*)(&As[kk][(lr * 4) ^ fk]);
-      const float4 b = *(const float4*)(&Bs[kk][(lc * 4) ^ fk]);
+      const float4 a = *(const float4*)(&As[ty][kk][(lr * 4) ^ fk]);
+      const float4 b = *(const float4*)(&Bs[ty][kk][(lc * 4) ^ fk]);
       acc[0][0] += a.x * b.x; acc[0][1] += a.x * b.y; acc[0][2] += a.x * b.z; acc[0][3] += a.x * b.w;
       acc[1][0] += a.y * b.x; acc[1][1] += a.y * b.y; acc[1][2] += a.y * b.z; acc[1][3] += a.y * b.w;
       acc[2][0] += a.z * b.x; acc[2][1] += a.z * b.y; acc[2][2] += a.z * b.z; acc[2][3] += a.z * b.w;
@@ -496,11 +568,11 @@
       const int n = bn + lc * 4 + j;
       const float v = acc[i][j] + kvb[(size_t)l * 2 * HID + n];
       if (n < 512) {
-        const int h = n >> 7, d = n & 127;
-        keys[(((size_t)l * NHD + h) * DKH + d) * LBN + m] = v;
+        const int hh = n >> 7, d = n & 127;
+        keys[(((size_t)l * NHD + hh) * DKH + d) * LBN + m] = v;
       } else {
-        const int c = n - 512, h = c >> 7, d = c & 127;
-        vals[(((size_t)l * NHD + h) * LBN + m) * DKH + d] = v;
+        const int c = n - 512, hh = c >> 7, d = c & 127;
+        vals[(((size_t)l * NHD + hh) * LBN + m) * DKH + d] = v;
       }
     }
   }
@@ -592,70 +664,70 @@
   const float alpha = 0.08838834764831845f;
   const long TH = (long)TT * HID;
   const long pz_ctx = (long)(ncho + 4) * 64 * DKH;
-
-  redln_k<<<TT, 256, 0, stream>>>(lfrm, HID, 1, nullptr, nullptr, 0,
-                                  n1g, n1b, lf, y1);
+  const dim3 B4(256, 4, 1);
+
+  redln_k<<<16, B4, 0, stream>>>(lfrm, HID, 1, nullptr, nullptr, 0,
+                                 n1g, n1b, lf, y1);
 
   for (int l = 0; l < LAY; ++l) {
     const float* Wkv = kvw + (size_t)l * HID * 2 * HID;
     const float* Bkv = kvbi + (size_t)l * 2 * HID;
     const float* qbi_l = qbi + (size_t)l * HID;
-    gemm_nn<<<dim3(32, 8, 1), 256, 0, stream>>>(
-        y1, HID, 0, w1 + (size_t)l * HID * FF, FF, 0, nullptr, 0, 0,
-        nullptr, nullptr, 0, FF, HID, 0, 8, part, 0, 0, 1, 0);
-    redln_k<<<TT, 256, 0, stream>>>(part, FF, 8, b1 + (size_t)l * FF, nullptr, 1,
-                                    fng + (size_t)l * FF, fnb + (size_t)l * FF,
-                                    nullptr, y2);
-    gemm_nn<<<dim3(8, 32, 1), 256, 0, stream>>>(
-        y2, FF, 0, w2 + (size_t)l * FF * HID, HID, 0, nullptr, 0, 0,
-        nullptr, nullptr, 0, HID, FF, 0, 32, part, 0, 0, 1, 0);
-    redln_k<<<TT, 256, 0, stream>>>(part, HID, 32, nullptr, nullptr, 0,
-                                    n2g + l * HID, n2b + l * HID, nullptr, y4);
-    fsmnln_k<<<TT, 256, 0, stream>>>(y4, lf, fcache + (size_t)l * HID * (KW - 1),
-                                     fw + (size_t)l * HID * KW,
-                                     n3g + l * HID, n3b + l * HID,
-                                     xb, out_fsmn + (size_t)l * HID * (KW - 1 + TT), y1);
-    gemm_nn<<<dim3(8, 8, 1), 256, 0, stream>>>(
-        y1, HID, 0, qw + (size_t)l * HID * HID, HID, 0, nullptr, 0, 0,
-        nullptr, nullptr, 0, HID, HID, 0, 8, part, 0, 0, 1, 0);
-    attn1_k<<<dim3(8 + ckv / 64, 1, NHD), 256, 0, stream>>>(
+    gemm_nn<<<dim3(32, 2, 1), B4, 0, stream>>>(
+        y1, HID, 0, w1 + (size_t)l * HID * FF, FF, 0, nullptr, 0, 0, nullptr,
+        FF, HID, 0, 8, part, 0, 0, 1, 0);
+    redln_k<<<16, B4, 0, stream>>>(part, FF, 8, b1 + (size_t)l * FF, nullptr, 1,
+                                   fng + (size_t)l * FF, fnb + (size_t)l * FF,
+                                   nullptr, y2);
+    gemm_nn<<<dim3(8, 8, 1), B4, 0, stream>>>(
+        y2, FF, 0, w2 + (size_t)l * FF * HID, HID, 0, nullptr, 0, 0, nullptr,
+        HID, FF, 0, 32, part, 0, 0, 1, 0);
+    redln_k<<<16, B4, 0, stream>>>(part, HID, 32, nullptr, nullptr, 0,
+                                   n2g + l * HID, n2b + l * HID, nullptr, y4);
+    fsmnln_k<<<16, B4, 0, stream>>>(y4, lf, fcache + (size_t)l * HID * (KW - 1),
+                                    fw + (size_t)l * HID * KW,
+                                    n3g + l * HID, n3b + l * HID,
+                                    xb, out_fsmn + (size_t)l * HID * (KW - 1 + TT), y1);
+    gemm_nn<<<dim3(8, 2, 1), B4, 0, stream>>>(
+        y1, HID, 0, qw + (size_t)l * HID * HID, HID, 0, nullptr, 0, 0, nullptr,
+        HID, HID, 0, 8, part, 0, 0, 1, 0);
+    attn1_k<<<dim3((8 + ckv / 64 + 3) / 4, 1, NHD), B4, 0, stream>>>(
         part, qbi_l, Wkv, kcache + (size_t)l * NHD * DKH * ckv, qp, sc, ckv, sct);
-    gemm_nt<<<dim3(32, 2, NHD), 256, 0, stream>>>(
+    gemm_nt<<<dim3(8, 2, NHD), B4, 0, stream>>>(
         qp, HID, TH, enc, HID, 0, sc + ckv, sct, TS, SEQ, HID, 2, partN);
-    softmax_k<<<NHD * TT, 256, 0, stream>>>(sc, rs, part, qbi_l, Bkv, partN,
-                                            sct, ckv, alpha);
-    attn2_k<<<dim3(10, 8, NHD), 256, 0, stream>>>(
+    softmax_k<<<64, B4, 0, stream>>>(sc, rs, part, qbi_l, Bkv, partN,
+                                     sct, ckv, alpha);
+    attn2_k<<<dim3(3, 8, NHD), B4, 0, stream>>>(
         sc, vcache + (size_t)l * NHD * ckv * DKH, enc, part, partE,
         ckv, sct, ncho, pz_ctx);
-    gemm_nn<<<dim3(2, 4, NHD), 256, 0, stream>>>(
+    gemm_nn<<<dim3(2, 1, NHD), B4, 0, stream>>>(
         partE, HID, 8L * 64 * HID, Wkv + HID, 2 * HID, DKH, nullptr, 0, 0,
-        nullptr, nullptr, 0, DKH, HID, 0, 4, part, pz_ctx, ncho, 8, 64L * HID);
-    red_k<<<128, 256, 0, stream>>>(part, ctx, DKH, ncho + 4, pz_ctx, HID, DKH,
-                                   nullptr, nullptr, rs, Bkv + HID, 0, NHD * TT * DKH);
-    gemm_nn<<<dim3(8, 8, 1), 256, 0, stream>>>(
-        ctx, HID, 0, ow + (size_t)l * HID * HID, HID, 0, nullptr, 0, 0,
-        nullptr, nullptr, 0, HID, HID, 0, 8, part, 0, 0, 1, 0);
+        nullptr, DKH, HID, 0, 4, part, pz_ctx, ncho, 8, 64L * HID);
+    red_k<<<32, 1024, 0, stream>>>(part, ctx, DKH, ncho + 4, pz_ctx, HID, DKH,
+                                   rs, Bkv + HID, NHD * TT * DKH);
+    gemm_nn<<<dim3(8, 2, 1), B4, 0, stream>>>(
+        ctx, HID, 0, ow + (size_t)l * HID * HID, HID, 0, nullptr, 0, 0, nullptr,
+        HID, HID, 0, 8, part, 0, 0, 1, 0);
     const float* ng = (l + 1 < LAY) ? n1g + (l + 1) * HID : d3n1g;
     const float* nb = (l + 1 < LAY) ? n1b + (l + 1) * HID : d3n1b;
-    redln_k<<<TT, 256, 0, stream>>>(part, HID, 8, obi + (size_t)l * HID, xb, 0,
-                                    ng, nb, lf, y1);
-  }
-
-  gemm_nn<<<dim3(32, 8, 1), 256, 0, stream>>>(
-      y1, HID, 0, d3w1, FF, 0, nullptr, 0, 0, nullptr, nullptr, 0,
+    redln_k<<<16, B4, 0, stream>>>(part, HID, 8, obi + (size_t)l * HID, xb, 0,
+                                   ng, nb, lf, y1);
+  }
+
+  gemm_nn<<<dim3(32, 2, 1), B4, 0, stream>>>(
+      y1, HID, 0, d3w1, FF, 0, nullptr, 0, 0, nullptr,
       FF, HID, 0, 8, part, 0, 0, 1, 0);
-  redln_k<<<TT, 256, 0, stream>>>(part, FF, 8, d3b1, nullptr, 1,
-                                  d3fng, d3fnb, nullptr, y2);
-  gemm_nn<<<dim3(8, 32, 1), 256, 0, stream>>>(
-      y2, FF, 0, d3w2, HID, 0, nullptr, 0, 0, nullptr, nullptr, 0,
+  redln_k<<<16, B4, 0, stream>>>(part, FF, 8, d3b1, nullptr, 1,
+                                 d3fng, d3fnb, nullptr, y2);
+  gemm_nn<<<dim3(8, 8, 1), B4, 0, stream>>>(
+      y2, FF, 0, d3w2, HID, 0, nullptr, 0, 0, nullptr,
       HID, FF, 0, 32, part, 0, 0, 1, 0);
-  redln_k<<<TT, 256, 0, stream>>>(part, HID, 32, nullptr, nullptr, 0,
-                                  ang, anb, nullptr, y4);
-  gemm_nn<<<dim3((VOC + 63) / 64, 1, 1), 256, 0, stream>>>(
-      y4, HID, 0, outw, VOC, 0, lg, VOC, 0, outb, nullptr, 0,
-      VOC, HID, 0, 1, nullptr, 0, 0, 1, 0);
-  argmax_k<<<TT, 256, 0, stream>>>(lg, out_ids);
-
-  kvsave_k<<<dim3(2 * HID / 64, LBN / 64, LAY), 256, 0, stream>>>(
+  redln_k<<<16, B4, 0, stream>>>(part, HID, 32, nullptr, nullptr, 0,
+                                 ang, anb, nullptr, y4);
+  gemm_vx<<<dim3(33, 1, 1), B4, 0, stream>>>(
+      y4, HID, outw, VOC, lg, VOC, outb, VOC, HID, (VOC + 63) / 64);
+  argmax_k<<<16, B4, 0, stream>>>(lg, out_ids);
+
+  kvsave_k<<<dim3(4, 4, 16), B4, 0, stream>>>(
       enc, kvw, kvbi, out_keys, out_vals);
 }
```

Result: slower. 4.556 ms (+51.1%).
